# Performance work log

Hardware: AMD Instinct MI355X
Metric: run time of the kernel (lower is better)

## Reference

```python
import jax, jax.numpy as jnp
import numpy as np

B = 8192
ID_DIM = 1024
LLM_DIM = 4096
IN_DIM = ID_DIM + LLM_DIM      # 5120
OUT_DIM = 2048
HID = OUT_DIM * 2              # 4096
E = 8
TOPK = 2
GATE_HID = E * 2               # 16


def setup_inputs() -> dict:
    key = jax.random.key(0)
    ks = jax.random.split(key, 12)
    s_in = 1.0 / np.sqrt(IN_DIM)
    s_hid = 1.0 / np.sqrt(HID)
    s_g = 1.0 / np.sqrt(GATE_HID)
    return {
        "id_emb": jax.random.normal(ks[0], (B, ID_DIM), jnp.float32),
        "llm_emb": jax.random.normal(ks[1], (B, LLM_DIM), jnp.float32),
        # stacked expert params
        "W1": jax.random.normal(ks[2], (E, IN_DIM, HID), jnp.float32) * s_in,
        "b1": jax.random.normal(ks[3], (E, HID), jnp.float32) * 0.01,
        "W2": jax.random.normal(ks[4], (E, HID, OUT_DIM), jnp.float32) * s_hid,
        "b2": jax.random.normal(ks[5], (E, OUT_DIM), jnp.float32) * 0.01,
        # gate params
        "gW1": jax.random.normal(ks[6], (IN_DIM, GATE_HID), jnp.float32) * s_in,
        "gb1": jax.random.normal(ks[7], (GATE_HID,), jnp.float32) * 0.01,
        "gW2": jax.random.normal(ks[8], (GATE_HID, E), jnp.float32) * s_g,
        "gb2": jax.random.normal(ks[9], (E,), jnp.float32) * 0.01,
    }


def reference(id_emb, llm_emb, W1, b1, W2, b2, gW1, gb1, gW2, gb2):
    combined = jnp.concatenate([id_emb, llm_emb], axis=-1)          # [B, IN]
    # gate: Linear -> ReLU -> Linear
    gate_logits = jax.nn.relu(combined @ gW1 + gb1) @ gW2 + gb2    # [B, E]
    topk_w, topk_i = jax.lax.top_k(gate_logits, TOPK)               # [B, K]
    topk_w = jax.nn.softmax(topk_w, axis=-1)
    # dense per-expert combine weights [B, E] (zero for non-selected experts)
    bsz = combined.shape[0]
    dense_w = jnp.zeros((bsz, E), combined.dtype).at[
        jnp.arange(bsz)[:, None], topk_i].add(topk_w)
    # dense all-experts MLP (faithful to reference: every expert on all tokens)
    h = jax.nn.relu(jnp.einsum('bi,eih->beh', combined, W1) + b1)  # [B, E, HID]
    expert_out = jnp.einsum('beh,eho->beo', h, W2) + b2            # [B, E, OUT]
    return jnp.einsum('be,beo->bo', dense_w, expert_out)           # [B, OUT]
```

## Files before the change

### kernel.cpp

```cpp
#include <hip/hip_runtime.h>
#include <hip/hip_bf16.h>
#include <hip/hip_fp16.h>

#define B_TOK 8192
#define ID_DIM 1024
#define LLM_DIM 4096
#define IN_DIM 5120
#define OUT_DIM 2048
#define HID 4096
#define NE 8
#define GH 16
#define NSLOT (2 * B_TOK)

#define NNT1 16
#define NKT1 80
#define NNT2 8
#define NKT2 64
#define MT256 72
#define GRID1B (MT256 * NNT1)
#define GRID2B (MT256 * NNT2)

typedef _Float16 f16x8 __attribute__((ext_vector_type(8)));
typedef float f32x4 __attribute__((ext_vector_type(4)));
typedef unsigned short u16;
typedef u16 u16x8 __attribute__((ext_vector_type(8)));

#define OFF_H   (1ull << 20)
#define OFF_X   (OFF_H + (size_t)NSLOT * HID * 2)
#define OFF_P1  (OFF_X + (size_t)B_TOK * IN_DIM * 2)
#define OFF_P2  (OFF_P1 + (size_t)NE * NNT1 * NKT1 * 32768)
#define REQ_WS  (OFF_P2 + (size_t)NE * NNT2 * NKT2 * 32768)
#define OFF_SLOT OFF_P1

#define INV_OFF 66560

__device__ __forceinline__ void gll16(void* lds, const void* gsrc) {
  __builtin_amdgcn_global_load_lds(
      (const __attribute__((address_space(1))) unsigned int*)gsrc,
      (__attribute__((address_space(3))) unsigned int*)lds, 16, 0, 0);
}

__global__ __launch_bounds__(256) void gate_kernel(
    const float* __restrict__ id_emb, const float* __restrict__ llm_emb,
    const float* __restrict__ gW1, const float* __restrict__ gb1,
    const float* __restrict__ gW2, const float* __restrict__ gb2,
    int* __restrict__ wsi, _Float16* __restrict__ xf16) {
  int wave = (blockIdx.x * blockDim.x + threadIdx.x) >> 6;
  int lane = threadIdx.x & 63;
  if (wave >= B_TOK) return;
  int b = wave;
  float acc[GH];
#pragma unroll
  for (int j = 0; j < GH; ++j) acc[j] = 0.f;
  for (int k = lane; k < IN_DIM; k += 64) {
    float x = (k < ID_DIM) ? id_emb[(size_t)b * ID_DIM + k]
                           : llm_emb[(size_t)b * LLM_DIM + (k - ID_DIM)];
    if (xf16) xf16[(size_t)b * IN_DIM + k] = (_Float16)x;
    const float* grow = gW1 + (size_t)k * GH;
#pragma unroll
    for (int j = 0; j < GH; ++j) acc[j] += x * grow[j];
  }
#pragma unroll
  for (int j = 0; j < GH; ++j) {
    for (int off = 32; off > 0; off >>= 1) acc[j] += __shfl_xor(acc[j], off);
  }
  if (lane == 0) {
    float logits[NE];
#pragma unroll
    for (int e = 0; e < NE; ++e) logits[e] = gb2[e];
#pragma unroll
    for (int j = 0; j < GH; ++j) {
      float hg = fmaxf(acc[j] + gb1[j], 0.f);
#pragma unroll
      for (int e = 0; e < NE; ++e) logits[e] += hg * gW2[j * NE + e];
    }
    int i0 = 0; float v0 = logits[0];
#pragma unroll
    for (int e = 1; e < NE; ++e) if (logits[e] > v0) { v0 = logits[e]; i0 = e; }
    int i1 = -1; float v1 = -1e30f;
#pragma unroll
    for (int e = 0; e < NE; ++e) if (e != i0 && logits[e] > v1) { v1 = logits[e]; i1 = e; }
    float ex = expf(v1 - v0);
    float w0 = 1.f / (1.f + ex);
    float w1 = ex / (1.f + ex);
    int* eidx = wsi + 1024;
    float* wsl = (float*)(wsi + 17408);
    eidx[b * 2] = i0; eidx[b * 2 + 1] = i1;
    wsl[b * 2] = w0; wsl[b * 2 + 1] = w1;
    atomicAdd(&wsi[i0], 1);
    atomicAdd(&wsi[i1], 1);
  }
}

__global__ void schedule_kernel(int* __restrict__ wsi) {
  if (threadIdx.x != 0 || blockIdx.x != 0) return;
  int* counts = wsi; int* cursor = wsi + 8;
  int* te = wsi + 16; int* tm = wsi + 272; int* tc = wsi + 528;
  int off = 0, t = 0;
  for (int e = 0; e < NE; ++e) {
    int c = counts[e];
    cursor[e] = off;
    int nt = (c + 255) >> 8;
    for (int i = 0; i < nt; ++i) {
      te[t] = e; tm[t] = off + i * 256;
      int rem = c - i * 256;
      tc[t] = rem < 256 ? rem : 256;
      ++t;
    }
    off += c;
  }
  for (; t < MT256; ++t) { te[t] = 0; tm[t] = 0; tc[t] = 0; }
}

__global__ __launch_bounds__(256) void scatter_kernel(int* __restrict__ wsi) {
  int s = blockIdx.x * blockDim.x + threadIdx.x;
  if (s >= NSLOT) return;
  int* cursor = wsi + 8;
  const int* eidx = wsi + 1024;
  const float* wsl = (const float*)(wsi + 17408);
  int* rows = wsi + 33792;
  float* wsorted = (float*)(wsi + 50176);
  int* inv = wsi + INV_OFF;
  int e = eidx[s];
  int pos = atomicAdd(&cursor[e], 1);
  rows[pos] = s;
  wsorted[pos] = wsl[s];
  inv[s] = pos;
}

__global__ __launch_bounds__(256) void pack_w(
    const float* __restrict__ W, _Float16* __restrict__ P,
    int N, int NNT, int NKT) {
  int kt = blockIdx.x, nt = blockIdx.y, e = blockIdx.z;
  const float* src = W + ((size_t)e * NKT * 64 + (size_t)kt * 64) * N + nt * 256;
  _Float16* dst = P + (((size_t)e * NNT + nt) * NKT + kt) * 16384;
  int t = threadIdx.x;
  int l = t & 63, sbb = t >> 6;
  int fr = l & 15, kg = l >> 4;
  for (int i = 0; i < 8; ++i) {
    int sb = sbb * 8 + i;
    int gn = sb >> 1, hh = sb & 1;
    const float* s = src + (size_t)(hh * 32 + kg * 8) * N + gn * 16 + fr;
    union { u16x8 u; _Float16 f[8]; } cv;
#pragma unroll
    for (int j = 0; j < 8; ++j) cv.f[j] = (_Float16)s[(size_t)j * N];
    *(u16x8*)(dst + gn * 1024 + hh * 512 + l * 8) = cv.u;
  }
}

#define SBAR __builtin_amdgcn_s_barrier()
#define SCHB __builtin_amdgcn_sched_barrier(0)
#define LGKM0 asm volatile("s_waitcnt lgkmcnt(0)" ::: "memory")

#define MFMA16(MH, H)                                                          \
  __builtin_amdgcn_s_setprio(1);                                               \
  _Pragma("unroll") for (int m = 0; m < 4; ++m)                                \
      _Pragma("unroll") for (int n = 0; n < 4; ++n)                            \
          acc[(MH)*4 + m][n] = __builtin_amdgcn_mfma_f32_16x16x32_f16(         \
              a[m], bfr[H][n], acc[(MH)*4 + m][n], 0, 0, 0);                   \
  __builtin_amdgcn_s_setprio(0);                                               \
  SCHB;

#define RD_A(MH, H)                                                            \
  _Pragma("unroll") for (int m = 0; m < 4; ++m)                                \
      a[m] = *(const f16x8*)(Ac + (wr * 8 + (MH)*4 + m) * 1024 + (H)*512 + lane * 8);
#define RD_B(H)                                                                \
  _Pragma("unroll") for (int n = 0; n < 4; ++n)                                \
      bfr[H][n] = *(const f16x8*)(Bc + (wc * 4 + n) * 1024 + (H)*512 + lane * 8);

#define ST_B(dstB, kt_, gn_, h_) \
  gll16((dstB) + (gn_)*1024 + (h_)*512, pb + (size_t)(kt_)*16384 + (gn_)*1024 + (h_)*512)
#define ST_A(dstA, kt_, pa_, gm_, h_) \
  gll16((dstA) + (gm_)*1024 + (h_)*512, (pa_) + (size_t)(kt_)*64 + (h_)*32)

#define GEMM_LOOP(NKT)                                                         \
  ST_B(B0, 0, gnA, 0); ST_B(B0, 0, gnA, 1);                                    \
  ST_B(B0, 0, gnB, 0); ST_B(B0, 0, gnB, 1);                                    \
  ST_A(A0, 0, paA, gm_a, 0); ST_A(A0, 0, paA, gm_a, 1);                        \
  ST_A(A0, 0, paB, gm_b, 0); ST_A(A0, 0, paB, gm_b, 1);                        \
  asm volatile("s_waitcnt vmcnt(2)" ::: "memory"); SCHB; SBAR;                 \
  for (int t = 0; t < (NKT); ++t) {                                            \
    _Float16* Ac = (t & 1) ? A1 : A0;                                          \
    _Float16* Bc = (t & 1) ? B1 : B0;                                          \
    _Float16* An = (t & 1) ? A0 : A1;                                          \
    _Float16* Bn = (t & 1) ? B0 : B1;                                          \
    bool stg = (t + 1 < (NKT));                                                \
    int k1 = t + 1;                                                            \
    f16x8 a[4]; f16x8 bfr[2][4];                                               \
                                                               \
    RD_A(0, 0) RD_B(0)                                                         \
    if (stg) { ST_B(Bn, k1, gnA, 0); ST_B(Bn, k1, gnA, 1); }                   \
    SBAR; LGKM0; SCHB;                                                         \
    MFMA16(0, 0) SBAR;                                                         \
                                                               \
    RD_A(0, 1) RD_B(1)                                                         \
    if (stg) {                                                                 \
      ST_B(Bn, k1, gnB, 0); ST_B(Bn, k1, gnB, 1);                              \
      asm volatile("s_waitcnt vmcnt(4)" ::: "memory");                         \
    } else {                                                                   \
      asm volatile("s_waitcnt vmcnt(0)" ::: "memory");                         \
    }                                                                          \
    SCHB; SBAR; LGKM0; SCHB;                                                   \
    MFMA16(0, 1) SBAR;                                                         \
                                                               \
    RD_A(1, 0)                                                                 \
    if (stg) { ST_A(An, k1, paA, gm_a, 0); ST_A(An, k1, paA, gm_a, 1); }       \
    SBAR; LGKM0; SCHB;                                                         \
    MFMA16(1, 0) SBAR;                                                         \
                                                               \
    RD_A(1, 1)                                                                 \
    if (stg) { ST_A(An, k1, paB, gm_b, 0); ST_A(An, k1, paB, gm_b, 1); }       \
    asm volatile("s_waitcnt vmcnt(2)" ::: "memory"); SCHB;                     \
    SBAR; LGKM0; SCHB;                                                         \
    MFMA16(1, 1) SBAR;                                                         \
  }

__global__ __launch_bounds__(512, 2) void gemm1_kernel(
    const _Float16* __restrict__ Xf, const _Float16* __restrict__ P1,
    const float* __restrict__ b1, const int* __restrict__ wsi,
    _Float16* __restrict__ hbuf) {
  __shared__ _Float16 smem[65536];
  int d = blockIdx.x;
  int orig = (d & 7) * (GRID1B >> 3) + (d >> 3);
  int tile = orig / NNT1;
  int nt = orig % NNT1;
  int cnt = (wsi + 528)[tile];
  if (cnt == 0) return;
  int e = (wsi + 16)[tile];
  int m0 = (wsi + 272)[tile];
  const int* rows = wsi + 33792;
  int n0 = nt * 256;
  int tid = threadIdx.x, lane = tid & 63, w = tid >> 6;
  int wr = w >> 2, wc = w & 3;
  int fr = lane & 15, kg = lane >> 4;

  int gm_a = wr * 8 + (w & 3);
  int gm_b = gm_a + 4;
  int gnA = w * 2, gnB = w * 2 + 1;
  int ra = gm_a * 16 + fr; ra = ra < cnt ? ra : cnt - 1;
  int rb = gm_b * 16 + fr; rb = rb < cnt ? rb : cnt - 1;
  const _Float16* paA = Xf + (size_t)(rows[m0 + ra] >> 1) * IN_DIM + kg * 8;
  const _Float16* paB = Xf + (size_t)(rows[m0 + rb] >> 1) * IN_DIM + kg * 8;
  const _Float16* pb = P1 + ((size_t)e * NNT1 + nt) * ((size_t)NKT1 * 16384) + lane * 8;

  _Float16* A0 = smem;
  _Float16* A1 = smem + 16384;
  _Float16* B0 = smem + 32768;
  _Float16* B1 = smem + 49152;

  f32x4 acc[8][4];
#pragma unroll
  for (int m = 0; m < 8; ++m)
#pragma unroll
    for (int n = 0; n < 4; ++n) acc[m][n] = (f32x4){0.f, 0.f, 0.f, 0.f};

  GEMM_LOOP(NKT1)

  float bias_n[4];
#pragma unroll
  for (int n = 0; n < 4; ++n) bias_n[n] = b1[e * HID + n0 + wc * 64 + n * 16 + fr];

  _Float16* ep = smem;
#pragma unroll
  for (int hh = 0; hh < 2; ++hh) {
    __syncthreads();
    if (wr == hh) {
#pragma unroll
      for (int m = 0; m < 8; ++m)
#pragma unroll
        for (int n = 0; n < 4; ++n)
#pragma unroll
          for (int r2 = 0; r2 < 4; ++r2) {
            int row_loc = m * 16 + kg * 4 + r2;
            int col_loc = wc * 64 + n * 16 + fr;
            ep[row_loc * 264 + col_loc] = (_Float16)fmaxf(acc[m][n][r2] + bias_n[n], 0.f);
          }
    }
    __syncthreads();
#pragma unroll
    for (int i = 0; i < 8; ++i) {
      int chunk = i * 512 + tid;
      int row = chunk >> 5, c16 = chunk & 31;
      int r = hh * 128 + row;
      if (r < cnt)
        *(u16x8*)&hbuf[(size_t)(m0 + r) * HID + n0 + c16 * 8] =
            *(const u16x8*)&ep[row * 264 + c16 * 8];
    }
  }
}

__global__ __launch_bounds__(512, 2) void gemm2_kernel(
    const _Float16* __restrict__ hbuf, const _Float16* __restrict__ P2,
    const float* __restrict__ b2, const int* __restrict__ wsi,
    float* __restrict__ slotbuf) {
  __shared__ _Float16 smem[65536];
  int d = blockIdx.x;
  int orig = (d & 7) * (GRID2B >> 3) + (d >> 3);
  int tile = orig / NNT2;
  int nt = orig % NNT2;
  int cnt = (wsi + 528)[tile];
  if (cnt == 0) return;
  int e = (wsi + 16)[tile];
  int m0 = (wsi + 272)[tile];
  const float* wsorted = (const float*)(wsi + 50176);
  int n0 = nt * 256;
  int tid = threadIdx.x, lane = tid & 63, w = tid >> 6;
  int wr = w >> 2, wc = w & 3;
  int fr = lane & 15, kg = lane >> 4;

  int gm_a = wr * 8 + (w & 3);
  int gm_b = gm_a + 4;
  int gnA = w * 2, gnB = w * 2 + 1;
  int ra = gm_a * 16 + fr; ra = ra < cnt ? ra : cnt - 1;
  int rb = gm_b * 16 + fr; rb = rb < cnt ? rb : cnt - 1;
  const _Float16* paA = hbuf + (size_t)(m0 + ra) * HID + kg * 8;
  const _Float16* paB = hbuf + (size_t)(m0 + rb) * HID + kg * 8;
  const _Float16* pb = P2 + ((size_t)e * NNT2 + nt) * ((size_t)NKT2 * 16384) + lane * 8;

  _Float16* A0 = smem;
  _Float16* A1 = smem + 16384;
  _Float16* B0 = smem + 32768;
  _Float16* B1 = smem + 49152;

  f32x4 acc[8][4];
#pragma unroll
  for (int m = 0; m < 8; ++m)
#pragma unroll
    for (int n = 0; n < 4; ++n) acc[m][n] = (f32x4){0.f, 0.f, 0.f, 0.f};

  GEMM_LOOP(NKT2)

  float bias_n[4];
#pragma unroll
  for (int n = 0; n < 4; ++n) bias_n[n] = b2[e * OUT_DIM + n0 + wc * 64 + n * 16 + fr];

#pragma unroll
  for (int m = 0; m < 8; ++m) {
#pragma unroll
    for (int r2 = 0; r2 < 4; ++r2) {
      int r = wr * 128 + m * 16 + kg * 4 + r2;
      if (r < cnt) {
        float wgt = wsorted[m0 + r];
        float* orow = slotbuf + (size_t)(m0 + r) * OUT_DIM + n0;
#pragma unroll
        for (int n = 0; n < 4; ++n)
          orow[wc * 64 + n * 16 + fr] = (acc[m][n][r2] + bias_n[n]) * wgt;
      }
    }
  }
}

__global__ __launch_bounds__(256) void combine_kernel(
    const float* __restrict__ slotbuf, const int* __restrict__ wsi,
    float* __restrict__ out) {
  int idx = blockIdx.x * 256 + threadIdx.x;
  int b = idx >> 9, c4 = (idx & 511) * 4;
  const int* inv = wsi + INV_OFF;
  int p0 = inv[b * 2], p1 = inv[b * 2 + 1];
  float4 a = *(const float4*)&slotbuf[(size_t)p0 * OUT_DIM + c4];
  float4 c = *(const float4*)&slotbuf[(size_t)p1 * OUT_DIM + c4];
  float4 o; o.x = a.x + c.x; o.y = a.y + c.y; o.z = a.z + c.z; o.w = a.w + c.w;
  *(float4*)&out[(size_t)b * OUT_DIM + c4] = o;
}

#define FB_MAX_TILES 136
__global__ void schedule_fb(int* __restrict__ wsi) {
  if (threadIdx.x != 0 || blockIdx.x != 0) return;
  int* counts = wsi; int* cursor = wsi + 8;
  int* te = wsi + 16; int* tm = wsi + 272; int* tc = wsi + 528;
  int off = 0, t = 0;
  for (int e = 0; e < NE; ++e) {
    int c = counts[e];
    cursor[e] = off;
    int nt = (c + 127) >> 7;
    for (int i = 0; i < nt; ++i) {
      te[t] = e; tm[t] = off + i * 128;
      int rem = c - i * 128;
      tc[t] = rem < 128 ? rem : 128;
      ++t;
    }
    off += c;
  }
  for (; t < FB_MAX_TILES; ++t) { te[t] = 0; tm[t] = 0; tc[t] = 0; }
}

__global__ __launch_bounds__(256, 2) void gemm1_fb(
    const float* __restrict__ id_emb, const float* __restrict__ llm_emb,
    const float* __restrict__ W1, const float* __restrict__ b1,
    const int* __restrict__ wsi, _Float16* __restrict__ h) {
  const int* te = wsi + 16; const int* tm = wsi + 272; const int* tc = wsi + 528;
  const int* rows = wsi + 33792;
  int tile = blockIdx.x;
  int cnt = tc[tile];
  if (cnt == 0) return;
  int e = te[tile], m0 = tm[tile];
  int n0 = blockIdx.y * 128;
  const float* Wb = W1 + (size_t)e * IN_DIM * HID;
  __shared__ _Float16 As[128][40];
  __shared__ _Float16 Bs[128][40];
  int tid = threadIdx.x;
  int lane = tid & 63, w = tid >> 6;
  int wr = w >> 1, wc = w & 1;
  int fr = lane & 15, kg = lane >> 4;
  f32x4 acc[4][4];
#pragma unroll
  for (int m = 0; m < 4; ++m)
#pragma unroll
    for (int n = 0; n < 4; ++n) acc[m][n] = (f32x4){0.f, 0.f, 0.f, 0.f};
  int a_ks = (tid & 3) * 8;
  int a_r = tid >> 2;
  int brow[2];
#pragma unroll
  for (int i = 0; i < 2; ++i) {
    int r = a_r + i * 64;
    brow[i] = (r < cnt) ? (rows[m0 + r] >> 1) : -1;
  }
  int b_c = tid & 127, b_kq = tid >> 7;
  for (int kt = 0; kt < IN_DIM; kt += 32) {
#pragma unroll
    for (int i = 0; i < 2; ++i) {
      int r = a_r + i * 64;
      float v[8];
      if (brow[i] >= 0) {
        int k = kt + a_ks;
        const float* src = (k < ID_DIM)
            ? (id_emb + (size_t)brow[i] * ID_DIM + k)
            : (llm_emb + (size_t)brow[i] * LLM_DIM + (k - ID_DIM));
        float4 v0 = *(const float4*)src;
        float4 v1 = *(const float4*)(src + 4);
        v[0] = v0.x; v[1] = v0.y; v[2] = v0.z; v[3] = v0.w;
        v[4] = v1.x; v[5] = v1.y; v[6] = v1.z; v[7] = v1.w;
      } else {
#pragma unroll
        for (int j = 0; j < 8; ++j) v[j] = 0.f;
      }
      union { u16x8 u; _Float16 f[8]; } cv;
#pragma unroll
      for (int j = 0; j < 8; ++j) cv.f[j] = (_Float16)v[j];
      *reinterpret_cast<u16x8*>(&As[r][a_ks]) = cv.u;
    }
#pragma unroll
    for (int i = 0; i < 2; ++i) {
      int kc = b_kq + i * 2;
      int k0 = kt + kc * 8;
      union { u16x8 u; _Float16 f[8]; } cv;
#pragma unroll
      for (int j = 0; j < 8; ++j)
        cv.f[j] = (_Float16)Wb[(size_t)(k0 + j) * HID + n0 + b_c];
      *reinterpret_cast<u16x8*>(&Bs[b_c][kc * 8]) = cv.u;
    }
    __syncthreads();
    f16x8 af[4], bf[4];
#pragma unroll
    for (int m = 0; m < 4; ++m)
      af[m] = *reinterpret_cast<const f16x8*>(&As[wr * 64 + m * 16 + fr][kg * 8]);
#pragma unroll
    for (int n = 0; n < 4; ++n)
      bf[n] = *reinterpret_cast<const f16x8*>(&Bs[wc * 64 + n * 16 + fr][kg * 8]);
#pragma unroll
    for (int m = 0; m < 4; ++m)
#pragma unroll
      for (int n = 0; n < 4; ++n)
        acc[m][n] = __builtin_amdgcn_mfma_f32_16x16x32_f16(af[m], bf[n], acc[m][n], 0, 0, 0);
    __syncthreads();
  }
#pragma unroll
  for (int m = 0; m < 4; ++m) {
    int rbv = wr * 64 + m * 16 + kg * 4;
#pragma unroll
    for (int n = 0; n < 4; ++n) {
      int col = n0 + wc * 64 + n * 16 + fr;
      float bias = b1[e * HID + col];
#pragma unroll
      for (int r2 = 0; r2 < 4; ++r2) {
        int r = rbv + r2;
        if (r < cnt) {
          float v = fmaxf(acc[m][n][r2] + bias, 0.f);
          h[(size_t)(m0 + r) * HID + col] = (_Float16)v;
        }
      }
    }
  }
}

__global__ __launch_bounds__(256, 2) void gemm2_fb(
    const _Float16* __restrict__ h, const float* __restrict__ W2,
    const float* __restrict__ b2, const int* __restrict__ wsi,
    float* __restrict__ out) {
  const int* te = wsi + 16; const int* tm = wsi + 272; const int* tc = wsi + 528;
  const int* rows = wsi + 33792;
  const float* wsorted = (const float*)(wsi + 50176);
  int tile = blockIdx.x;
  int cnt = tc[tile];
  if (cnt == 0) return;
  int e = te[tile], m0 = tm[tile];
  int n0 = blockIdx.y * 128;
  const float* Wb = W2 + (size_t)e * HID * OUT_DIM;
  __shared__ _Float16 As[128][40];
  __shared__ _Float16 Bs[128][40];
  int tid = threadIdx.x;
  int lane = tid & 63, w = tid >> 6;
  int wr = w >> 1, wc = w & 1;
  int fr = lane & 15, kg = lane >> 4;
  f32x4 acc[4][4];
#pragma unroll
  for (int m = 0; m < 4; ++m)
#pragma unroll
    for (int n = 0; n < 4; ++n) acc[m][n] = (f32x4){0.f, 0.f, 0.f, 0.f};
  int a_ks = (tid & 3) * 8;
  int a_r = tid >> 2;
  int b_c = tid & 127, b_kq = tid >> 7;
  for (int kt = 0; kt < HID; kt += 32) {
#pragma unroll
    for (int i = 0; i < 2; ++i) {
      int r = a_r + i * 64;
      u16x8 v;
      if (r < cnt) {
        v = *reinterpret_cast<const u16x8*>(&h[(size_t)(m0 + r) * HID + kt + a_ks]);
      } else {
        v = (u16x8){0, 0, 0, 0, 0, 0, 0, 0};
      }
      *reinterpret_cast<u16x8*>(&As[r][a_ks]) = v;
    }
#pragma unroll
    for (int i = 0; i < 2; ++i) {
      int kc = b_kq + i * 2;
      int k0 = kt + kc * 8;
      union { u16x8 u; _Float16 f[8]; } cv;
#pragma unroll
      for (int j = 0; j < 8; ++j)
        cv.f[j] = (_Float16)Wb[(size_t)(k0 + j) * OUT_DIM + n0 + b_c];
      *reinterpret_cast<u16x8*>(&Bs[b_c][kc * 8]) = cv.u;
    }
    __syncthreads();
    f16x8 af[4], bf[4];
#pragma unroll
    for (int m = 0; m < 4; ++m)
      af[m] = *reinterpret_cast<const f16x8*>(&As[wr * 64 + m * 16 + fr][kg * 8]);
#pragma unroll
    for (int n = 0; n < 4; ++n)
      bf[n] = *reinterpret_cast<const f16x8*>(&Bs[wc * 64 + n * 16 + fr][kg * 8]);
#pragma unroll
    for (int m = 0; m < 4; ++m)
#pragma unroll
      for (int n = 0; n < 4; ++n)
        acc[m][n] = __builtin_amdgcn_mfma_f32_16x16x32_f16(af[m], bf[n], acc[m][n], 0, 0, 0);
    __syncthreads();
  }
#pragma unroll
  for (int m = 0; m < 4; ++m) {
    int rbv = wr * 64 + m * 16 + kg * 4;
#pragma unroll
    for (int n = 0; n < 4; ++n) {
      int col = n0 + wc * 64 + n * 16 + fr;
      float bias = b2[e * OUT_DIM + col];
#pragma unroll
      for (int r2 = 0; r2 < 4; ++r2) {
        int r = rbv + r2;
        if (r < cnt) {
          int slot = rows[m0 + r];
          int btok = slot >> 1;
          float wgt = wsorted[m0 + r];
          atomicAdd(&out[(size_t)btok * OUT_DIM + col], (acc[m][n][r2] + bias) * wgt);
        }
      }
    }
  }
}

extern "C" void kernel_launch(void* const* d_in, const int* in_sizes, int n_in,
                              void* d_out, int out_size, void* d_ws, size_t ws_size,
                              hipStream_t stream) {
  const float* id_emb  = (const float*)d_in[0];
  const float* llm_emb = (const float*)d_in[1];
  const float* W1  = (const float*)d_in[2];
  const float* b1  = (const float*)d_in[3];
  const float* W2  = (const float*)d_in[4];
  const float* b2  = (const float*)d_in[5];
  const float* gW1 = (const float*)d_in[6];
  const float* gb1 = (const float*)d_in[7];
  const float* gW2 = (const float*)d_in[8];
  const float* gb2 = (const float*)d_in[9];
  float* out = (float*)d_out;
  int* wsi = (int*)d_ws;
  _Float16* h = (_Float16*)((char*)d_ws + OFF_H);
  bool fast = ws_size >= REQ_WS;

  hipMemsetAsync(d_ws, 0, 4096, stream);

  if (fast) {
    _Float16* xf = (_Float16*)((char*)d_ws + OFF_X);
    _Float16* p1 = (_Float16*)((char*)d_ws + OFF_P1);
    _Float16* p2 = (_Float16*)((char*)d_ws + OFF_P2);
    float* slotbuf = (float*)((char*)d_ws + OFF_SLOT);
    gate_kernel<<<B_TOK / 4, 256, 0, stream>>>(id_emb, llm_emb, gW1, gb1, gW2, gb2, wsi, xf);
    schedule_kernel<<<1, 64, 0, stream>>>(wsi);
    scatter_kernel<<<NSLOT / 256, 256, 0, stream>>>(wsi);
    pack_w<<<dim3(NKT1, NNT1, NE), 256, 0, stream>>>(W1, p1, HID, NNT1, NKT1);
    pack_w<<<dim3(NKT2, NNT2, NE), 256, 0, stream>>>(W2, p2, OUT_DIM, NNT2, NKT2);
    gemm1_kernel<<<GRID1B, 512, 0, stream>>>(xf, p1, b1, wsi, h);
    gemm2_kernel<<<GRID2B, 512, 0, stream>>>(h, p2, b2, wsi, slotbuf);
    combine_kernel<<<(B_TOK * OUT_DIM / 4) / 256, 256, 0, stream>>>(slotbuf, wsi, out);
  } else {
    hipMemsetAsync(d_out, 0, (size_t)B_TOK * OUT_DIM * sizeof(float), stream);
    gate_kernel<<<B_TOK / 4, 256, 0, stream>>>(id_emb, llm_emb, gW1, gb1, gW2, gb2, wsi, nullptr);
    schedule_fb<<<1, 64, 0, stream>>>(wsi);
    scatter_kernel<<<NSLOT / 256, 256, 0, stream>>>(wsi);
    gemm1_fb<<<dim3(FB_MAX_TILES, 32), 256, 0, stream>>>(id_emb, llm_emb, W1, b1, wsi, h);
    gemm2_fb<<<dim3(FB_MAX_TILES, 16), 256, 0, stream>>>(h, W2, b2, wsi, out);
  }
}
```

Baseline: 2.056 ms.

## Switch GEMM mainloop to 4-stage K=32 LDS ring with 3-deep prefetch

Replaces the double-buffered K=64 pipeline with a four-slot ring of K=32 stages in the same 64K-half LDS footprint, keeping three stages of global-to-LDS loads in flight. Weight packing is changed to match the 32-wide K slabs. The aim is to hide global latency better with a deeper prefetch. In exchange it runs twice as many iterations with more barriers per unit of MFMA work, and the B fragments are reused across two M halves.

```diff
diff --git a/kernel.cpp b/kernel.cpp
--- a/kernel.cpp
+++ b/kernel.cpp
@@ -13,9 +13,9 @@
 #define NSLOT (2 * B_TOK)
 
 #define NNT1 16
-#define NKT1 80
+#define NKS1 160
 #define NNT2 8
-#define NKT2 64
+#define NKS2 128
 #define MT256 72
 #define GRID1B (MT256 * NNT1)
 #define GRID2B (MT256 * NNT2)
@@ -28,8 +28,8 @@
 #define OFF_H   (1ull << 20)
 #define OFF_X   (OFF_H + (size_t)NSLOT * HID * 2)
 #define OFF_P1  (OFF_X + (size_t)B_TOK * IN_DIM * 2)
-#define OFF_P2  (OFF_P1 + (size_t)NE * NNT1 * NKT1 * 32768)
-#define REQ_WS  (OFF_P2 + (size_t)NE * NNT2 * NKT2 * 32768)
+#define OFF_P2  (OFF_P1 + (size_t)NE * NNT1 * NKS1 * 16384)
+#define REQ_WS  (OFF_P2 + (size_t)NE * NNT2 * NKS2 * 16384)
 #define OFF_SLOT OFF_P1
 
 #define INV_OFF 66560
@@ -130,89 +130,77 @@
 
 __global__ __launch_bounds__(256) void pack_w(
     const float* __restrict__ W, _Float16* __restrict__ P,
-    int N, int NNT, int NKT) {
-  int kt = blockIdx.x, nt = blockIdx.y, e = blockIdx.z;
-  const float* src = W + ((size_t)e * NKT * 64 + (size_t)kt * 64) * N + nt * 256;
-  _Float16* dst = P + (((size_t)e * NNT + nt) * NKT + kt) * 16384;
+    int N, int NNT, int NKS) {
+  int ks = blockIdx.x, nt = blockIdx.y, e = blockIdx.z;
+  const float* src = W + ((size_t)e * NKS * 32 + (size_t)ks * 32) * N + nt * 256;
+  _Float16* dst = P + (((size_t)e * NNT + nt) * NKS + ks) * 8192;
   int t = threadIdx.x;
-  int l = t & 63, sbb = t >> 6;
+  int l = t & 63, q = t >> 6;
   int fr = l & 15, kg = l >> 4;
-  for (int i = 0; i < 8; ++i) {
-    int sb = sbb * 8 + i;
-    int gn = sb >> 1, hh = sb & 1;
-    const float* s = src + (size_t)(hh * 32 + kg * 8) * N + gn * 16 + fr;
+  for (int gn = q; gn < 16; gn += 4) {
+    const float* s = src + (size_t)(kg * 8) * N + gn * 16 + fr;
     union { u16x8 u; _Float16 f[8]; } cv;
 #pragma unroll
     for (int j = 0; j < 8; ++j) cv.f[j] = (_Float16)s[(size_t)j * N];
-    *(u16x8*)(dst + gn * 1024 + hh * 512 + l * 8) = cv.u;
+    *(u16x8*)(dst + gn * 512 + l * 8) = cv.u;
   }
 }
 
 #define SBAR __builtin_amdgcn_s_barrier()
 #define SCHB __builtin_amdgcn_sched_barrier(0)
 #define LGKM0 asm volatile("s_waitcnt lgkmcnt(0)" ::: "memory")
-
-#define MFMA16(MH, H)                                                          \
-  __builtin_amdgcn_s_setprio(1);                                               \
-  _Pragma("unroll") for (int m = 0; m < 4; ++m)                                \
+#define VMW(n) asm volatile("s_waitcnt vmcnt(" #n ")" ::: "memory")
+
+#define ST_A(Aw, ks_, pa_, gm_) gll16((Aw) + (gm_) * 512, (pa_) + (size_t)(ks_) * 32)
+#define ST_B(Bw, ks_, gn_) \
+  gll16((Bw) + (gn_) * 512, pb + (size_t)(ks_) * 8192 + (gn_) * 512)
+
+#define GEMM_LOOP(NKS)                                                         \
+  {                                                                            \
+    _Pragma("unroll") for (int kp = 0; kp < 3; ++kp) {                         \
+      _Float16* Aw = smem + kp * 8192;                                         \
+      _Float16* Bw = smem + 32768 + kp * 8192;                                 \
+      ST_A(Aw, kp, paA, gm_a); ST_A(Aw, kp, paB, gm_b);                        \
+      ST_B(Bw, kp, gnA); ST_B(Bw, kp, gnB);                                    \
+    }                                                                          \
+    VMW(8); SCHB; SBAR;                                                        \
+    for (int k = 0; k < (NKS); ++k) {                                          \
+      int rb = k & 3, wbi = (k + 3) & 3;                                       \
+      _Float16* Ac = smem + rb * 8192;                                         \
+      _Float16* Bc = smem + 32768 + rb * 8192;                                 \
+      _Float16* Aw = smem + wbi * 8192;                                        \
+      _Float16* Bw = smem + 32768 + wbi * 8192;                                \
+      f16x8 a[4], b4[4];                                                       \
+                                          \
+      _Pragma("unroll") for (int m = 0; m < 4; ++m)                            \
+          a[m] = *(const f16x8*)(Ac + (wr * 8 + m) * 512 + lane * 8);          \
       _Pragma("unroll") for (int n = 0; n < 4; ++n)                            \
-          acc[(MH)*4 + m][n] = __builtin_amdgcn_mfma_f32_16x16x32_f16(         \
-              a[m], bfr[H][n], acc[(MH)*4 + m][n], 0, 0, 0);                   \
-  __builtin_amdgcn_s_setprio(0);                                               \
-  SCHB;
-
-#define RD_A(MH, H)                                                            \
-  _Pragma("unroll") for (int m = 0; m < 4; ++m)                                \
-      a[m] = *(const f16x8*)(Ac + (wr * 8 + (MH)*4 + m) * 1024 + (H)*512 + lane * 8);
-#define RD_B(H)                                                                \
-  _Pragma("unroll") for (int n = 0; n < 4; ++n)                                \
-      bfr[H][n] = *(const f16x8*)(Bc + (wc * 4 + n) * 1024 + (H)*512 + lane * 8);
-
-#define ST_B(dstB, kt_, gn_, h_) \
-  gll16((dstB) + (gn_)*1024 + (h_)*512, pb + (size_t)(kt_)*16384 + (gn_)*1024 + (h_)*512)
-#define ST_A(dstA, kt_, pa_, gm_, h_) \
-  gll16((dstA) + (gm_)*1024 + (h_)*512, (pa_) + (size_t)(kt_)*64 + (h_)*32)
-
-#define GEMM_LOOP(NKT)                                                         \
-  ST_B(B0, 0, gnA, 0); ST_B(B0, 0, gnA, 1);                                    \
-  ST_B(B0, 0, gnB, 0); ST_B(B0, 0, gnB, 1);                                    \
-  ST_A(A0, 0, paA, gm_a, 0); ST_A(A0, 0, paA, gm_a, 1);                        \
-  ST_A(A0, 0, paB, gm_b, 0); ST_A(A0, 0, paB, gm_b, 1);                        \
-  asm volatile("s_waitcnt vmcnt(2)" ::: "memory"); SCHB; SBAR;                 \
-  for (int t = 0; t < (NKT); ++t) {                                            \
-    _Float16* Ac = (t & 1) ? A1 : A0;                                          \
-    _Float16* Bc = (t & 1) ? B1 : B0;                                          \
-    _Float16* An = (t & 1) ? A0 : A1;                                          \
-    _Float16* Bn = (t & 1) ? B0 : B1;                                          \
-    bool stg = (t + 1 < (NKT));                                                \
-    int k1 = t + 1;                                                            \
-    f16x8 a[4]; f16x8 bfr[2][4];                                               \
-                                                               \
-    RD_A(0, 0) RD_B(0)                                                         \
-    if (stg) { ST_B(Bn, k1, gnA, 0); ST_B(Bn, k1, gnA, 1); }                   \
-    SBAR; LGKM0; SCHB;                                                         \
-    MFMA16(0, 0) SBAR;                                                         \
-                                                               \
-    RD_A(0, 1) RD_B(1)                                                         \
-    if (stg) {                                                                 \
-      ST_B(Bn, k1, gnB, 0); ST_B(Bn, k1, gnB, 1);                              \
-      asm volatile("s_waitcnt vmcnt(4)" ::: "memory");                         \
-    } else {                                                                   \
-      asm volatile("s_waitcnt vmcnt(0)" ::: "memory");                         \
+          b4[n] = *(const f16x8*)(Bc + (wc * 4 + n) * 512 + lane * 8);         \
+      if (k + 3 < (NKS)) {                                                     \
+        ST_A(Aw, k + 3, paA, gm_a); ST_A(Aw, k + 3, paB, gm_b);                \
+        ST_B(Bw, k + 3, gnA); ST_B(Bw, k + 3, gnB);                            \
+      }                                                                        \
+      SBAR; LGKM0; SCHB;                                                       \
+      __builtin_amdgcn_s_setprio(1);                                           \
+      _Pragma("unroll") for (int m = 0; m < 4; ++m)                            \
+          _Pragma("unroll") for (int n = 0; n < 4; ++n)                        \
+              acc[m][n] = __builtin_amdgcn_mfma_f32_16x16x32_f16(              \
+                  a[m], b4[n], acc[m][n], 0, 0, 0);                            \
+      __builtin_amdgcn_s_setprio(0); SCHB; SBAR;                               \
+                          \
+      _Pragma("unroll") for (int m = 0; m < 4; ++m)                            \
+          a[m] = *(const f16x8*)(Ac + (wr * 8 + 4 + m) * 512 + lane * 8);      \
+      if (k < (NKS) - 3) { VMW(8); }                                           \
+      else if (k == (NKS) - 3) { VMW(4); }                                     \
+      else if (k == (NKS) - 2) { VMW(0); }                                     \
+      SCHB; SBAR; LGKM0; SCHB;                                                 \
+      __builtin_amdgcn_s_setprio(1);                                           \
+      _Pragma("unroll") for (int m = 0; m < 4; ++m)                            \
+          _Pragma("unroll") for (int n = 0; n < 4; ++n)                        \
+              acc[4 + m][n] = __builtin_amdgcn_mfma_f32_16x16x32_f16(          \
+                  a[m], b4[n], acc[4 + m][n], 0, 0, 0);                        \
+      __builtin_amdgcn_s_setprio(0); SCHB; SBAR;                               \
     }                                                                          \
-    SCHB; SBAR; LGKM0; SCHB;                                                   \
-    MFMA16(0, 1) SBAR;                                                         \
-                                                               \
-    RD_A(1, 0)                                                                 \
-    if (stg) { ST_A(An, k1, paA, gm_a, 0); ST_A(An, k1, paA, gm_a, 1); }       \
-    SBAR; LGKM0; SCHB;                                                         \
-    MFMA16(1, 0) SBAR;                                                         \
-                                                               \
-    RD_A(1, 1)                                                                 \
-    if (stg) { ST_A(An, k1, paB, gm_b, 0); ST_A(An, k1, paB, gm_b, 1); }       \
-    asm volatile("s_waitcnt vmcnt(2)" ::: "memory"); SCHB;                     \
-    SBAR; LGKM0; SCHB;                                                         \
-    MFMA16(1, 1) SBAR;                                                         \
   }
 
 __global__ __launch_bounds__(512, 2) void gemm1_kernel(
@@ -238,15 +226,10 @@
   int gm_b = gm_a + 4;
   int gnA = w * 2, gnB = w * 2 + 1;
   int ra = gm_a * 16 + fr; ra = ra < cnt ? ra : cnt - 1;
-  int rb = gm_b * 16 + fr; rb = rb < cnt ? rb : cnt - 1;
+  int rb2 = gm_b * 16 + fr; rb2 = rb2 < cnt ? rb2 : cnt - 1;
   const _Float16* paA = Xf + (size_t)(rows[m0 + ra] >> 1) * IN_DIM + kg * 8;
-  const _Float16* paB = Xf + (size_t)(rows[m0 + rb] >> 1) * IN_DIM + kg * 8;
-  const _Float16* pb = P1 + ((size_t)e * NNT1 + nt) * ((size_t)NKT1 * 16384) + lane * 8;
-
-  _Float16* A0 = smem;
-  _Float16* A1 = smem + 16384;
-  _Float16* B0 = smem + 32768;
-  _Float16* B1 = smem + 49152;
+  const _Float16* paB = Xf + (size_t)(rows[m0 + rb2] >> 1) * IN_DIM + kg * 8;
+  const _Float16* pb = P1 + ((size_t)e * NNT1 + nt) * ((size_t)NKS1 * 8192) + lane * 8;
 
   f32x4 acc[8][4];
 #pragma unroll
@@ -254,7 +237,7 @@
 #pragma unroll
     for (int n = 0; n < 4; ++n) acc[m][n] = (f32x4){0.f, 0.f, 0.f, 0.f};
 
-  GEMM_LOOP(NKT1)
+  GEMM_LOOP(NKS1)
 
   float bias_n[4];
 #pragma unroll
@@ -312,15 +295,10 @@
   int gm_b = gm_a + 4;
   int gnA = w * 2, gnB = w * 2 + 1;
   int ra = gm_a * 16 + fr; ra = ra < cnt ? ra : cnt - 1;
-  int rb = gm_b * 16 + fr; rb = rb < cnt ? rb : cnt - 1;
+  int rb2 = gm_b * 16 + fr; rb2 = rb2 < cnt ? rb2 : cnt - 1;
   const _Float16* paA = hbuf + (size_t)(m0 + ra) * HID + kg * 8;
-  const _Float16* paB = hbuf + (size_t)(m0 + rb) * HID + kg * 8;
-  const _Float16* pb = P2 + ((size_t)e * NNT2 + nt) * ((size_t)NKT2 * 16384) + lane * 8;
-
-  _Float16* A0 = smem;
-  _Float16* A1 = smem + 16384;
-  _Float16* B0 = smem + 32768;
-  _Float16* B1 = smem + 49152;
+  const _Float16* paB = hbuf + (size_t)(m0 + rb2) * HID + kg * 8;
+  const _Float16* pb = P2 + ((size_t)e * NNT2 + nt) * ((size_t)NKS2 * 8192) + lane * 8;
 
   f32x4 acc[8][4];
 #pragma unroll
@@ -328,7 +306,7 @@
 #pragma unroll
     for (int n = 0; n < 4; ++n) acc[m][n] = (f32x4){0.f, 0.f, 0.f, 0.f};
 
-  GEMM_LOOP(NKT2)
+  GEMM_LOOP(NKS2)
 
   float bias_n[4];
 #pragma unroll
@@ -596,8 +574,8 @@
     gate_kernel<<<B_TOK / 4, 256, 0, stream>>>(id_emb, llm_emb, gW1, gb1, gW2, gb2, wsi, xf);
     schedule_kernel<<<1, 64, 0, stream>>>(wsi);
     scatter_kernel<<<NSLOT / 256, 256, 0, stream>>>(wsi);
-    pack_w<<<dim3(NKT1, NNT1, NE), 256, 0, stream>>>(W1, p1, HID, NNT1, NKT1);
-    pack_w<<<dim3(NKT2, NNT2, NE), 256, 0, stream>>>(W2, p2, OUT_DIM, NNT2, NKT2);
+    pack_w<<<dim3(NKS1, NNT1, NE), 256, 0, stream>>>(W1, p1, HID, NNT1, NKS1);
+    pack_w<<<dim3(NKS2, NNT2, NE), 256, 0, stream>>>(W2, p2, OUT_DIM, NNT2, NKS2);
     gemm1_kernel<<<GRID1B, 512, 0, stream>>>(xf, p1, b1, wsi, h);
     gemm2_kernel<<<GRID2B, 512, 0, stream>>>(h, p2, b2, wsi, slotbuf);
     combine_kernel<<<(B_TOK * OUT_DIM / 4) / 256, 256, 0, stream>>>(slotbuf, wsi, out);
```

Result: faster. 1.933 ms (-6.0%).
